# Optimization experiments

Hardware: AMD Instinct MI355X
Metric: run time of the kernel (lower is better)

The kernel has to match this reference:

```python
import jax, jax.numpy as jnp
import numpy as np

N_NODES = 100000
N_EDGES = 1600000
N_GRAPHS = 1024
NODE_F = 100
HID = 64
GLOB_F = 3


def setup_inputs() -> dict:
    key = jax.random.key(0)
    ks = jax.random.split(key, 16)
    s = 0.05
    return {
        "x": jax.random.normal(ks[0], (N_NODES, NODE_F), dtype=jnp.float32),
        "edge_index": jax.random.randint(ks[1], (2, N_EDGES), 0, N_NODES, dtype=jnp.int32),
        "batch": jnp.sort(jax.random.randint(ks[2], (N_NODES,), 0, N_GRAPHS, dtype=jnp.int32)),
        "global_features": jax.random.normal(ks[3], (N_GRAPHS, GLOB_F), dtype=jnp.float32),
        "W1": jax.random.normal(ks[4], (NODE_F, HID), dtype=jnp.float32) * s,
        "b1": jnp.zeros((HID,), dtype=jnp.float32),
        "W2": jax.random.normal(ks[5], (HID, HID), dtype=jnp.float32) * s,
        "b2": jnp.zeros((HID,), dtype=jnp.float32),
        "gW1": jax.random.normal(ks[6], (GLOB_F, HID), dtype=jnp.float32) * s,
        "gb1": jnp.zeros((HID,), dtype=jnp.float32),
        "gW2": jax.random.normal(ks[7], (HID, HID), dtype=jnp.float32) * s,
        "gb2": jnp.zeros((HID,), dtype=jnp.float32),
        "cW1": jax.random.normal(ks[8], (2 * HID, HID), dtype=jnp.float32) * s,
        "cb1": jnp.zeros((HID,), dtype=jnp.float32),
        "cW2": jax.random.normal(ks[9], (HID, 1), dtype=jnp.float32) * s,
        "cb2": jnp.zeros((1,), dtype=jnp.float32),
    }


def gcn_conv(x, src, dst, W, b):
    # PyG GCNConv: add self-loops, symmetric degree normalization, linear transform.
    n = x.shape[0]
    loop = jnp.arange(n, dtype=src.dtype)
    src_sl = jnp.concatenate([src, loop])
    dst_sl = jnp.concatenate([dst, loop])
    deg = jax.ops.segment_sum(jnp.ones_like(dst_sl, dtype=x.dtype), dst_sl, num_segments=n)
    dinv = deg ** -0.5  # deg >= 1 due to self-loops
    norm = dinv[src_sl] * dinv[dst_sl]  # [E+N]
    h = x @ W  # [N, HID]
    msg = h[src_sl] * norm[:, None]
    out = jax.ops.segment_sum(msg, dst_sl, num_segments=n)
    return out + b


def reference(x, edge_index, batch, global_features,
              W1, b1, W2, b2, gW1, gb1, gW2, gb2, cW1, cb1, cW2, cb2):
    src, dst = edge_index[0], edge_index[1]
    h = jax.nn.relu(gcn_conv(x, src, dst, W1, b1))
    # dropout p=0.2 is identity in eval mode
    h = gcn_conv(h, src, dst, W2, b2)
    # global mean pool over graph ids
    sums = jax.ops.segment_sum(h, batch, num_segments=N_GRAPHS)
    cnts = jax.ops.segment_sum(jnp.ones((h.shape[0],), h.dtype), batch, num_segments=N_GRAPHS)
    pooled = sums / jnp.maximum(cnts, 1.0)[:, None]  # [G, HID]
    g = jax.nn.relu(global_features @ gW1 + gb1) @ gW2 + gb2  # [G, HID]
    combined = jnp.concatenate([pooled, g], axis=1)  # [G, 2*HID]
    out = jax.nn.relu(combined @ cW1 + cb1) @ cW2 + cb2  # [G, 1]
    return out
```

## Files before the change

kernel.cpp:

```cpp
#include <hip/hip_runtime.h>

#define N_NODES  100000
#define N_EDGES  1600000
#define N_GRAPHS 1024
#define NODE_F   100
#define HID      64
#define GLOB_F   3

#define CAP      64

#define P_PART     8
#define W_PART     1024
#define R_PART     ((N_NODES + P_PART - 1) / P_PART)
#define CHUNK_PART ((N_EDGES + W_PART - 1) / W_PART)

typedef _Float16 half_t;
typedef __attribute__((ext_vector_type(8))) _Float16 half8;

__global__ void k_bucket(const int* __restrict__ src, const int* __restrict__ dst,
                         int* __restrict__ cnt, int* __restrict__ csrc_pad, int E) {
    int p = blockIdx.x % P_PART;
    int w = blockIdx.x / P_PART;
    int lo_node = p * R_PART;
    int start = w * CHUNK_PART;
    int end = start + CHUNK_PART; if (end > E) end = E;
    for (int i = start + (int)threadIdx.x; i < end; i += 256) {
        int d = dst[i];
        if ((unsigned)(d - lo_node) < (unsigned)R_PART) {
            int pos = atomicAdd(&cnt[d], 1);
            if (pos < CAP) csrc_pad[((size_t)d << 6) + pos] = src[i];
        }
    }
}

template <int K, int SCALE>
__launch_bounds__(256, 3)
__global__ void k_mm(const float* __restrict__ X, const float* __restrict__ W,
                     const int* __restrict__ cnt, half_t* __restrict__ Y, int N) {
    __shared__ float Xs[16 * K];
    __shared__ float dsh[16];
    int tid = threadIdx.x;
    int row0 = blockIdx.x * 16;

    const float4* Xg = reinterpret_cast<const float4*>(X + (size_t)row0 * K);
    float4* Xls = reinterpret_cast<float4*>(Xs);
    for (int i = tid; i < 16 * K / 4; i += 256) Xls[i] = Xg[i];
    if (SCALE && tid < 16) dsh[tid] = 1.0f / sqrtf((float)(1 + cnt[row0 + tid]));

    int lane = tid & 63;
    int wv = tid >> 6;

    float Wr[K];
#pragma unroll
    for (int k = 0; k < K; ++k) Wr[k] = W[k * HID + lane];
    __syncthreads();

#pragma unroll
    for (int rr = 0; rr < 4; ++rr) {
        int r = row0 + wv * 4 + rr;
        const float4* xrow = reinterpret_cast<const float4*>(&Xs[(wv * 4 + rr) * K]);
        float acc0 = 0.f, acc1 = 0.f, acc2 = 0.f, acc3 = 0.f;
#pragma unroll
        for (int k4 = 0; k4 < K / 4; ++k4) {
            float4 xv = xrow[k4];
            acc0 += xv.x * Wr[k4 * 4 + 0];
            acc1 += xv.y * Wr[k4 * 4 + 1];
            acc2 += xv.z * Wr[k4 * 4 + 2];
            acc3 += xv.w * Wr[k4 * 4 + 3];
        }
        float acc = (acc0 + acc1) + (acc2 + acc3);
        if (SCALE) acc *= dsh[wv * 4 + rr];
        Y[(size_t)r * HID + lane] = (half_t)acc;
    }
}

template <int RELU, int SRCSCALE>
__global__ void k_gather(const half_t* __restrict__ Hs, const int* __restrict__ cnt,
                         const int* __restrict__ csrc_pad,
                         const float* __restrict__ b, float* __restrict__ outbuf, int N) {
    int tid = threadIdx.x;
    int d = blockIdx.x * 4 + (tid >> 6);
    if (d >= N) return;
    int lane = tid & 63;
    int g = lane >> 3;
    int l = lane & 7;
    int deg = cnt[d];
    int n = deg < CAP ? deg : CAP;
    const int* row = csrc_pad + ((size_t)d << 6);

    float acc[8] = {0, 0, 0, 0, 0, 0, 0, 0};

    int e = 0;
    for (; e + 16 <= n; e += 16) {
        int s0 = row[e + g];
        int s1 = row[e + 8 + g];
        float w0 = 1.0f, w1 = 1.0f;
        if (SRCSCALE) {
            w0 = 1.0f / sqrtf((float)(1 + cnt[s0]));
            w1 = 1.0f / sqrtf((float)(1 + cnt[s1]));
        }
        half8 h0 = *reinterpret_cast<const half8*>(Hs + (size_t)s0 * HID + l * 8);
        half8 h1 = *reinterpret_cast<const half8*>(Hs + (size_t)s1 * HID + l * 8);
#pragma unroll
        for (int j = 0; j < 8; ++j) acc[j] += w0 * (float)h0[j];
#pragma unroll
        for (int j = 0; j < 8; ++j) acc[j] += w1 * (float)h1[j];
    }
    for (; e < n; e += 8) {
        int ee = e + g;
        if (ee < n) {
            int s = row[ee];
            float ws = SRCSCALE ? (1.0f / sqrtf((float)(1 + cnt[s]))) : 1.0f;
            half8 hv = *reinterpret_cast<const half8*>(Hs + (size_t)s * HID + l * 8);
#pragma unroll
            for (int j = 0; j < 8; ++j) acc[j] += ws * (float)hv[j];
        }
    }
    if (g == 0) {
        float wd = SRCSCALE ? (1.0f / sqrtf((float)(1 + deg))) : 1.0f;
        half8 hv = *reinterpret_cast<const half8*>(Hs + (size_t)d * HID + l * 8);
#pragma unroll
        for (int j = 0; j < 8; ++j) acc[j] += wd * (float)hv[j];
    }
#pragma unroll
    for (int off = 8; off <= 32; off <<= 1) {
#pragma unroll
        for (int j = 0; j < 8; ++j) acc[j] += __shfl_xor(acc[j], off);
    }

    if (g == 0) {
        float dd = 1.0f / sqrtf((float)(1 + deg));
        float v[8];
#pragma unroll
        for (int j = 0; j < 8; ++j) {
            v[j] = acc[j] * dd + b[l * 8 + j];
            if (RELU) v[j] = fmaxf(v[j], 0.0f);
        }
        float4* o = reinterpret_cast<float4*>(outbuf + (size_t)d * HID + l * 8);
        o[0] = make_float4(v[0], v[1], v[2], v[3]);
        o[1] = make_float4(v[4], v[5], v[6], v[7]);
    }
}

__global__ void k_poolhead(const float* __restrict__ H, const int* __restrict__ batch,
                           const float* __restrict__ gf,
                           const float* __restrict__ gW1, const float* __restrict__ gb1,
                           const float* __restrict__ gW2, const float* __restrict__ gb2,
                           const float* __restrict__ cW1, const float* __restrict__ cb1,
                           const float* __restrict__ cW2, const float* __restrict__ cb2,
                           float* __restrict__ out, int N) {
    int g = blockIdx.x;
    __shared__ int sh_lo, sh_hi;
    __shared__ float red[4][HID];
    __shared__ float comb[2 * HID];
    if (threadIdx.x == 0) {
        int lo = 0, hi = N;
        while (lo < hi) { int m = (lo + hi) >> 1; if (batch[m] < g) lo = m + 1; else hi = m; }
        sh_lo = lo;
        int lo2 = lo, hi2 = N;
        while (lo2 < hi2) { int m = (lo2 + hi2) >> 1; if (batch[m] < g + 1) lo2 = m + 1; else hi2 = m; }
        sh_hi = lo2;
    }
    __syncthreads();
    int lo = sh_lo, hi = sh_hi;
    int wave = threadIdx.x >> 6, lane = threadIdx.x & 63;
    float acc = 0.0f;
    for (int i = lo + wave; i < hi; i += 4)
        acc += H[(size_t)i * HID + lane];
    red[wave][lane] = acc;
    __syncthreads();

    if (wave == 0) {
        float s = red[0][lane] + red[1][lane] + red[2][lane] + red[3][lane];
        int c = hi - lo;
        comb[lane] = s / (float)(c > 0 ? c : 1);

        float a = gb1[lane];
#pragma unroll
        for (int k = 0; k < GLOB_F; ++k) a += gf[g * GLOB_F + k] * gW1[k * HID + lane];
        float gh = fmaxf(a, 0.0f);
        float a2 = gb2[lane];
#pragma unroll 8
        for (int k = 0; k < HID; ++k) a2 += __shfl(gh, k) * gW2[k * HID + lane];
        comb[HID + lane] = a2;

        float a3 = cb1[lane];
#pragma unroll 8
        for (int k = 0; k < 2 * HID; ++k) a3 += comb[k] * cW1[k * HID + lane];
        a3 = fmaxf(a3, 0.0f);

        float prod = a3 * cW2[lane];
#pragma unroll
        for (int off = 32; off > 0; off >>= 1) prod += __shfl_down(prod, off);
        if (lane == 0) out[g] = prod + cb2[0];
    }
}

extern "C" void kernel_launch(void* const* d_in, const int* in_sizes, int n_in,
                              void* d_out, int out_size, void* d_ws, size_t ws_size,
                              hipStream_t stream) {
    const float* x     = (const float*)d_in[0];
    const int*   ei    = (const int*)d_in[1];
    const int*   batch = (const int*)d_in[2];
    const float* gf    = (const float*)d_in[3];
    const float* W1    = (const float*)d_in[4];
    const float* b1    = (const float*)d_in[5];
    const float* W2    = (const float*)d_in[6];
    const float* b2    = (const float*)d_in[7];
    const float* gW1   = (const float*)d_in[8];
    const float* gb1   = (const float*)d_in[9];
    const float* gW2   = (const float*)d_in[10];
    const float* gb2   = (const float*)d_in[11];
    const float* cW1   = (const float*)d_in[12];
    const float* cb1   = (const float*)d_in[13];
    const float* cW2   = (const float*)d_in[14];
    const float* cb2   = (const float*)d_in[15];
    float* out = (float*)d_out;

    const int* src = ei;
    const int* dst = ei + N_EDGES;

    char* w = (char*)d_ws;
    half_t* Hs       = (half_t*)w; w += (size_t)N_NODES * HID * sizeof(half_t);
    float*  bufB     = (float*)w;  w += (size_t)N_NODES * HID * sizeof(float);
    int*    cnt      = (int*)w;    w += (size_t)N_NODES * sizeof(int);
    int*    csrc_pad = (int*)w;    w += (size_t)N_NODES * CAP * sizeof(int);

    const int BT = 256;

    hipMemsetAsync(cnt, 0, (size_t)N_NODES * sizeof(int), stream);
    k_bucket<<<P_PART * W_PART, BT, 0, stream>>>(src, dst, cnt, csrc_pad, N_EDGES);

    k_mm<NODE_F, 0><<<N_NODES / 16, BT, 0, stream>>>(x, W1, cnt, Hs, N_NODES);
    k_gather<1, 1><<<(N_NODES + 3) / 4, BT, 0, stream>>>(Hs, cnt, csrc_pad, b1, bufB, N_NODES);

    k_mm<HID, 1><<<N_NODES / 16, BT, 0, stream>>>(bufB, W2, cnt, Hs, N_NODES);
    k_gather<0, 0><<<(N_NODES + 3) / 4, BT, 0, stream>>>(Hs, cnt, csrc_pad, b2, bufB, N_NODES);

    k_poolhead<<<N_GRAPHS, BT, 0, stream>>>(bufB, batch, gf, gW1, gb1, gW2, gb2,
                                            cW1, cb1, cW2, cb2, out, N_NODES);
}
```

Baseline: 259.7 us.

## Replace atomic edge bucketing with two-pass binned counting sort

Replaces the partitioned global-atomic bucketing of edges into padded per-node source lists with a counting sort. A per-block histogram over 256-node bins and a scan produce bin offsets, then edges are scattered into bins through shared memory. A per-bin pass fills the per-node lists using shared-memory atomics. This removes the memset and the heavy global atomics and redundant dst rescans, in exchange for extra kernel launches, a serial single-block scan, and an intermediate buffer aliased onto bufB.

```diff
diff --git a/kernel.cpp b/kernel.cpp
--- a/kernel.cpp
+++ b/kernel.cpp
@@ -9,28 +9,119 @@
 
 #define CAP      64
 
-#define P_PART     8
-#define W_PART     1024
-#define R_PART     ((N_NODES + P_PART - 1) / P_PART)
-#define CHUNK_PART ((N_EDGES + W_PART - 1) / W_PART)
+#define NBIN      391
+#define NBLK_BIN  256
+#define CHUNK_BIN (N_EDGES / NBLK_BIN)
 
 typedef _Float16 half_t;
 typedef __attribute__((ext_vector_type(8))) _Float16 half8;
 
-__global__ void k_bucket(const int* __restrict__ src, const int* __restrict__ dst,
-                         int* __restrict__ cnt, int* __restrict__ csrc_pad, int E) {
-    int p = blockIdx.x % P_PART;
-    int w = blockIdx.x / P_PART;
-    int lo_node = p * R_PART;
-    int start = w * CHUNK_PART;
-    int end = start + CHUNK_PART; if (end > E) end = E;
-    for (int i = start + (int)threadIdx.x; i < end; i += 256) {
-        int d = dst[i];
-        if ((unsigned)(d - lo_node) < (unsigned)R_PART) {
-            int pos = atomicAdd(&cnt[d], 1);
-            if (pos < CAP) csrc_pad[((size_t)d << 6) + pos] = src[i];
-        }
-    }
+__global__ void k_hist(const int* __restrict__ dst, int* __restrict__ hist_blk, int E) {
+    __shared__ int hist[NBIN];
+    int tid = threadIdx.x, blk = blockIdx.x;
+    for (int b = tid; b < NBIN; b += 256) hist[b] = 0;
+    __syncthreads();
+    int start = blk * CHUNK_BIN;
+    for (int i = start + tid; i < start + CHUNK_BIN; i += 256)
+        atomicAdd(&hist[dst[i] >> 8], 1);
+    __syncthreads();
+    for (int b = tid; b < NBIN; b += 256) hist_blk[blk * NBIN + b] = hist[b];
+}
+
+__global__ void k_scanb(const int* __restrict__ hist_blk, int* __restrict__ base_blk,
+                        int* __restrict__ bin_base) {
+    __shared__ int sc[512];
+    int t = threadIdx.x;
+    int total = 0;
+    if (t < NBIN) {
+        int run = 0;
+        for (int blk = 0; blk < NBLK_BIN; ++blk) {
+            int v = hist_blk[blk * NBIN + t];
+            base_blk[blk * NBIN + t] = run;
+            run += v;
+        }
+        total = run;
+    }
+    sc[t] = (t < NBIN) ? total : 0;
+    __syncthreads();
+    for (int off = 1; off < 512; off <<= 1) {
+        int o = (t >= off) ? sc[t - off] : 0;
+        __syncthreads();
+        sc[t] += o;
+        __syncthreads();
+    }
+    if (t < NBIN) bin_base[t] = sc[t] - total;
+    if (t == NBIN - 1) bin_base[NBIN] = sc[t];
+}
+
+__global__ void k_bin(const int* __restrict__ src, const int* __restrict__ dst,
+                      const int* __restrict__ bin_base, const int* __restrict__ base_blk,
+                      uint2* __restrict__ binned, int E) {
+    __shared__ int hist[NBIN];
+    __shared__ int lbase[NBIN];
+    __shared__ int lcur[NBIN];
+    __shared__ int gbl[NBIN];
+    __shared__ int scA[512], scB[512];
+    __shared__ uint2 pairs[CHUNK_BIN];
+
+    int tid = threadIdx.x, blk = blockIdx.x;
+    int start = blk * CHUNK_BIN;
+
+    for (int b = tid; b < NBIN; b += 256) hist[b] = 0;
+    __syncthreads();
+    for (int i = start + tid; i < start + CHUNK_BIN; i += 256)
+        atomicAdd(&hist[dst[i] >> 8], 1);
+    __syncthreads();
+
+    scA[tid] = (tid < NBIN) ? hist[tid] : 0;
+    scA[tid + 256] = (tid + 256 < NBIN) ? hist[tid + 256] : 0;
+    __syncthreads();
+    int* cur = scA; int* nxt = scB;
+    for (int off = 1; off < 512; off <<= 1) {
+        for (int j = tid; j < 512; j += 256)
+            nxt[j] = cur[j] + ((j >= off) ? cur[j - off] : 0);
+        __syncthreads();
+        int* tmp = cur; cur = nxt; nxt = tmp;
+    }
+    for (int b = tid; b < NBIN; b += 256) {
+        lbase[b] = cur[b] - hist[b];
+        lcur[b] = 0;
+        gbl[b] = bin_base[b] + base_blk[blk * NBIN + b];
+    }
+    __syncthreads();
+
+    for (int i = start + tid; i < start + CHUNK_BIN; i += 256) {
+        int d = dst[i]; int s = src[i];
+        int b = d >> 8;
+        int off = atomicAdd(&lcur[b], 1);
+        pairs[lbase[b] + off] = make_uint2((unsigned)s, (unsigned)d);
+    }
+    __syncthreads();
+
+    int wv = tid >> 6, lane = tid & 63;
+    for (int b = wv; b < NBIN; b += 4) {
+        int n = hist[b], lb = lbase[b], gb = gbl[b];
+        for (int j = lane; j < n; j += 64)
+            binned[gb + j] = pairs[lb + j];
+    }
+}
+
+__global__ void k_build(const uint2* __restrict__ binned, const int* __restrict__ bin_base,
+                        int* __restrict__ cnt, int* __restrict__ csrc_pad, int N) {
+    __shared__ int lcnt[256];
+    int b = blockIdx.x, tid = threadIdx.x;
+    int node_lo = b << 8;
+    lcnt[tid] = 0;
+    __syncthreads();
+    int lo = bin_base[b], hi = bin_base[b + 1];
+    for (int i = lo + tid; i < hi; i += 256) {
+        uint2 p = binned[i];
+        int pos = atomicAdd(&lcnt[p.y - node_lo], 1);
+        if (pos < CAP) csrc_pad[((size_t)p.y << 6) + pos] = (int)p.x;
+    }
+    __syncthreads();
+    int node = node_lo + tid;
+    if (node < N) cnt[node] = lcnt[tid];
 }
 
 template <int K, int SCALE>
@@ -225,11 +316,17 @@
     float*  bufB     = (float*)w;  w += (size_t)N_NODES * HID * sizeof(float);
     int*    cnt      = (int*)w;    w += (size_t)N_NODES * sizeof(int);
     int*    csrc_pad = (int*)w;    w += (size_t)N_NODES * CAP * sizeof(int);
+    int*    hist_blk = (int*)w;    w += (size_t)NBLK_BIN * NBIN * sizeof(int);
+    int*    base_blk = (int*)w;    w += (size_t)NBLK_BIN * NBIN * sizeof(int);
+    int*    bin_base = (int*)w;    w += (size_t)(NBIN + 1) * sizeof(int);
+    uint2*  binned   = (uint2*)bufB;
 
     const int BT = 256;
 
-    hipMemsetAsync(cnt, 0, (size_t)N_NODES * sizeof(int), stream);
-    k_bucket<<<P_PART * W_PART, BT, 0, stream>>>(src, dst, cnt, csrc_pad, N_EDGES);
+    k_hist<<<NBLK_BIN, BT, 0, stream>>>(dst, hist_blk, N_EDGES);
+    k_scanb<<<1, 512, 0, stream>>>(hist_blk, base_blk, bin_base);
+    k_bin<<<NBLK_BIN, BT, 0, stream>>>(src, dst, bin_base, base_blk, binned, N_EDGES);
+    k_build<<<NBIN, BT, 0, stream>>>(binned, bin_base, cnt, csrc_pad, N_NODES);
 
     k_mm<NODE_F, 0><<<N_NODES / 16, BT, 0, stream>>>(x, W1, cnt, Hs, N_NODES);
     k_gather<1, 1><<<(N_NODES + 3) / 4, BT, 0, stream>>>(Hs, cnt, csrc_pad, b1, bufB, N_NODES);
```

Result: faster. 248.6 us (-4.3%).
